# Kernel tuning notes

Measured on AMD Instinct MI355X. Metric: run time of the kernel, lower is better.

Reference implementation:

```python
import jax, jax.numpy as jnp
import numpy as np

N, E = 50000, 1600000
IN_F, OUT_F = 128, 128
T, B = 16, 8  # num_edge_types, num_bases
LN_EPS = 1e-5

def setup_inputs() -> dict:
    key = jax.random.key(0)
    ks = jax.random.split(key, 6)
    x = jax.random.normal(ks[0], (N, IN_F), dtype=jnp.float32)
    edge_index = jax.random.randint(ks[1], (2, E), 0, N, dtype=jnp.int64)
    edge_type = jax.random.randint(ks[2], (E,), 0, T, dtype=jnp.int64)
    edge_weight = jnp.ones((E,), dtype=jnp.float32)
    weight = jax.random.normal(ks[3], (B, IN_F, OUT_F), dtype=jnp.float32) * 0.05
    alpha = jax.random.normal(ks[4], (T, B), dtype=jnp.float32) * 0.05
    bias = jnp.zeros((OUT_F,), dtype=jnp.float32)
    w_self = jax.random.normal(ks[5], (IN_F, OUT_F), dtype=jnp.float32) * 0.05
    ln_gamma = jnp.ones((OUT_F,), dtype=jnp.float32)
    ln_beta = jnp.zeros((OUT_F,), dtype=jnp.float32)
    return {"x": x, "edge_index": edge_index, "edge_type": edge_type,
            "edge_weight": edge_weight, "weight": weight, "alpha": alpha,
            "bias": bias, "w_self": w_self, "ln_gamma": ln_gamma, "ln_beta": ln_beta}

def reference(x, edge_index, edge_type, edge_weight, weight, alpha, bias, w_self, ln_gamma, ln_beta):
    n = x.shape[0]
    row, col = edge_index[0], edge_index[1]
    # graph.row_norm(): normalize edge weights by destination-row weighted degree (full graph)
    deg = jax.ops.segment_sum(edge_weight, row, num_segments=n)
    norm_w = edge_weight / jnp.maximum(deg[row], 1e-12)
    # basis combination: W_t = sum_b alpha[t,b] * weight[b]
    W = jnp.einsum('tb,bio->tio', alpha, weight)            # [T, in, out]
    h_all = jnp.einsum('ni,tio->tno', x, W)                  # [T, N, out]
    # fused per-edge-type spmm: msg_e = norm_w_e * h_all[type_e, col_e], scatter-add to row_e
    msgs = h_all[edge_type, col] * norm_w[:, None]           # [E, out]
    h = jax.ops.segment_sum(msgs, row, num_segments=n)       # [N, out]
    # dropout is identity in eval mode; layer norm with affine params
    mu = jnp.mean(h, axis=-1, keepdims=True)
    var = jnp.mean((h - mu) ** 2, axis=-1, keepdims=True)
    h = (h - mu) * jax.lax.rsqrt(var + LN_EPS) * ln_gamma + ln_beta
    h = h + bias
    h = h + x @ w_self
    return h
```

## Files before the change

kernel.cpp:

```cpp
#include <hip/hip_runtime.h>

#define NT 16
#define NB 8
#define CAP 80
#define BUKCAP 8960
#define EPB 4096

typedef __attribute__((ext_vector_type(8))) short short8;
typedef __attribute__((ext_vector_type(4))) float f32x4;
typedef __attribute__((ext_vector_type(2))) float f32x2;

__device__ __forceinline__ unsigned short f2bf(float f) {
  unsigned int u = __float_as_uint(f);
  u += 0x7FFFu + ((u >> 16) & 1u);
  return (unsigned short)(u >> 16);
}
__device__ __forceinline__ unsigned int packbf2(float a, float b) {
  return (unsigned int)f2bf(a) | ((unsigned int)f2bf(b) << 16);
}

__device__ __forceinline__ f32x2 pk_mul(f32x2 a, f32x2 b) {
  f32x2 r;
  asm("v_pk_mul_f32 %0, %1, %2" : "=v"(r) : "v"(a), "v"(b));
  return r;
}
__device__ __forceinline__ void pk_fma_lo(f32x2& acc, f32x2 x, f32x2 c) {
  asm("v_pk_fma_f32 %0, %1, %2, %0 op_sel_hi:[1,0,1]" : "+v"(acc) : "v"(x), "v"(c));
}
__device__ __forceinline__ void pk_fma_hi(f32x2& acc, f32x2 x, f32x2 c) {
  asm("v_pk_fma_f32 %0, %1, %2, %0 op_sel:[0,1,0] op_sel_hi:[1,1,1]"
      : "+v"(acc) : "v"(x), "v"(c));
}

__device__ __forceinline__ void xprep_body(const float* __restrict__ x,
                                           unsigned short* __restrict__ xb, int i,
                                           int total8) {
  if (i < total8) {
    const float4* p = (const float4*)(x + (size_t)i * 8);
    float4 v0 = p[0], v1 = p[1];
    uint4 q = make_uint4(packbf2(v0.x, v0.y), packbf2(v0.z, v0.w),
                         packbf2(v1.x, v1.y), packbf2(v1.z, v1.w));
    *(uint4*)(xb + (size_t)i * 8) = q;
  }
}

__device__ __forceinline__ void wprep_body(const float* __restrict__ weight,
                                           const float* __restrict__ wself,
                                           unsigned short* __restrict__ WbB,
                                           unsigned short* __restrict__ wsB, int idx) {
  const int TOT = NB * 128 * 128;
  if (idx < TOT) {
    int b = idx >> 14, k = (idx >> 7) & 127, n = idx & 127;
    float s = weight[(size_t)(b * 128 + k) * 128 + n];
    int ct = n >> 4, n15 = n & 15, ks = k >> 5, lq = (k >> 3) & 3, j = k & 7;
    WbB[(size_t)((((b * 8 + ct) * 4 + ks) * 4 + lq) * 16 + n15) * 8 + j] = f2bf(s);
  } else if (idx < TOT + 128 * 128) {
    int i2 = idx - TOT;
    int k = i2 >> 7, n = i2 & 127;
    float s = wself[k * 128 + n];
    int ct = n >> 4, n15 = n & 15, ks = k >> 5, lq = (k >> 3) & 3, j = k & 7;
    wsB[((((ct * 4 + ks) * 4 + lq) * 16 + n15) * 8 + j)] = f2bf(s);
  }
}


__global__ __launch_bounds__(256) void k_part(
    const int* __restrict__ row, const int* __restrict__ col,
    const int* __restrict__ etype, const float* __restrict__ ew,
    int* __restrict__ gcount, int2* __restrict__ buk, const float* __restrict__ x,
    unsigned short* __restrict__ xb, const float* __restrict__ weight,
    const float* __restrict__ wself, unsigned short* __restrict__ WbB,
    unsigned short* __restrict__ wsB, int E, int N, int pb, int xbb) {
  int gb = blockIdx.x;
  if (gb < pb) {
    __shared__ int cnt[256];
    __shared__ int rbase[256];
    int base = gb * EPB;
    cnt[threadIdx.x] = 0;
    __syncthreads();
    int myb[16], myrank[16];
#pragma unroll
    for (int k = 0; k < 16; ++k) {
      int e = base + k * 256 + threadIdx.x;
      myb[k] = -1;
      myrank[k] = 0;
      if (e < E) {
        int r = row[e];
        int b = r >> 8;
        myb[k] = b | ((r & 255) << 8);
        myrank[k] = atomicAdd(&cnt[b], 1);
      }
    }
    __syncthreads();
    int c = cnt[threadIdx.x];
    rbase[threadIdx.x] = (c > 0) ? atomicAdd(&gcount[threadIdx.x], c) : 0;
    __syncthreads();
#pragma unroll
    for (int k = 0; k < 16; ++k) {
      if (myb[k] >= 0) {
        int e = base + k * 256 + threadIdx.x;
        int b = myb[k] & 255;
        int rl = (myb[k] >> 8) & 255;
        int pos = rbase[b] + myrank[k];
        if (pos < BUKCAP)
          buk[(size_t)b * BUKCAP + pos] =
              make_int2(col[e] | (etype[e] << 16) | (rl << 20), __float_as_int(ew[e]));
      }
    }
  } else if (gb < pb + xbb) {
    xprep_body(x, xb, (gb - pb) * 256 + threadIdx.x, N * 16);
  } else {
    wprep_body(weight, wself, WbB, wsB, (gb - pb - xbb) * 256 + threadIdx.x);
  }
}


__global__ __launch_bounds__(256) void k_bin(const int* __restrict__ gcount,
                                             const int2* __restrict__ buk,
                                             int* __restrict__ rcnt,
                                             int2* __restrict__ epk, int N) {
  __shared__ int cnt[256];
  int b = blockIdx.x;
  int n = gcount[b];
  if (n > BUKCAP) n = BUKCAP;
  cnt[threadIdx.x] = 0;
  __syncthreads();
  const int2* src = buk + (size_t)b * BUKCAP;
  for (int i = threadIdx.x; i < n; i += 256) {
    int2 rec = src[i];
    int lr = (rec.x >> 20) & 255;
    int pos = atomicAdd(&cnt[lr], 1);
    if (pos < CAP) {
      int grow = (b << 8) + lr;
      epk[(size_t)grow * CAP + pos] = make_int2(rec.x & 0xFFFFF, rec.y);
    }
  }
  __syncthreads();
  int grow = (b << 8) + threadIdx.x;
  if (grow < N) rcnt[grow] = min(cnt[threadIdx.x], CAP);
}


__global__ __launch_bounds__(256) void k_prep(
    const int* __restrict__ row, const int* __restrict__ col,
    const int* __restrict__ etype, const float* __restrict__ ew,
    int* __restrict__ rcnt, int2* __restrict__ epk, const float* __restrict__ x,
    unsigned short* __restrict__ xb, const float* __restrict__ weight,
    const float* __restrict__ wself, unsigned short* __restrict__ WbB,
    unsigned short* __restrict__ wsB, int E, int N, int eb, int xbb) {
  int gb = blockIdx.x;
  if (gb < eb) {
    int e0 = (gb * 256 + threadIdx.x) * 2;
    int e1 = e0 + 1;
    int r0 = -1, r1 = -1, pos0 = 0, pos1 = 0;
    if (e0 < E) { r0 = row[e0]; pos0 = atomicAdd(&rcnt[r0], 1); }
    if (e1 < E) { r1 = row[e1]; pos1 = atomicAdd(&rcnt[r1], 1); }
    if (r0 >= 0 && pos0 < CAP)
      epk[(size_t)r0 * CAP + pos0] = make_int2(col[e0] | (etype[e0] << 16),
                                               __float_as_int(ew[e0]));
    if (r1 >= 0 && pos1 < CAP)
      epk[(size_t)r1 * CAP + pos1] = make_int2(col[e1] | (etype[e1] << 16),
                                               __float_as_int(ew[e1]));
  } else if (gb < eb + xbb) {
    xprep_body(x, xb, (gb - eb) * 256 + threadIdx.x, N * 16);
  } else {
    wprep_body(weight, wself, WbB, wsB, (gb - eb - xbb) * 256 + threadIdx.x);
  }
}


__global__ void k_xprep(const float* __restrict__ x, unsigned short* __restrict__ xb,
                        int total8) {
  xprep_body(x, xb, blockIdx.x * 256 + threadIdx.x, total8);
}

__global__ void k_wprep(const float* __restrict__ weight, const float* __restrict__ wself,
                        unsigned short* __restrict__ WbB,
                        unsigned short* __restrict__ wselfB) {
  wprep_body(weight, wself, WbB, wselfB, blockIdx.x * 256 + threadIdx.x);
}

__global__ void k_count(const int* __restrict__ row, int* __restrict__ cnt, int E) {
  int e = blockIdx.x * blockDim.x + threadIdx.x;
  if (e < E) atomicAdd(&cnt[row[e]], 1);
}

__global__ __launch_bounds__(256) void k_scan_local(const int* __restrict__ cnt,
                                                    int* __restrict__ rstart,
                                                    int* __restrict__ bsum, int n) {
  __shared__ int ws[4];
  int tid = threadIdx.x;
  int i = blockIdx.x * 256 + tid;
  int lane = tid & 63, w = tid >> 6;
  int v = (i < n) ? cnt[i] : 0;
  int s = v;
#pragma unroll
  for (int d = 1; d < 64; d <<= 1) {
    int t = __shfl_up(s, d);
    if (lane >= d) s += t;
  }
  if (lane == 63) ws[w] = s;
  __syncthreads();
  int add = 0;
  for (int j = 0; j < w; ++j) add += ws[j];
  if (i < n) rstart[i] = s + add - v;
  if (tid == 255) bsum[blockIdx.x] = s + add;
}

__global__ __launch_bounds__(256) void k_scan_small(const int* __restrict__ bsum,
                                                    int* __restrict__ bsumx, int nb) {
  __shared__ int ws[4];
  int tid = threadIdx.x;
  int lane = tid & 63, w = tid >> 6;
  int v = (tid < nb) ? bsum[tid] : 0;
  int s = v;
#pragma unroll
  for (int d = 1; d < 64; d <<= 1) {
    int t = __shfl_up(s, d);
    if (lane >= d) s += t;
  }
  if (lane == 63) ws[w] = s;
  __syncthreads();
  int add = 0;
  for (int j = 0; j < w; ++j) add += ws[j];
  if (tid < nb) bsumx[tid] = s + add - v;
}

__global__ void k_scan_add(int* __restrict__ rstart, int* __restrict__ nxt,
                           const int* __restrict__ bsumx, int n) {
  int i = blockIdx.x * 256 + threadIdx.x;
  if (i < n) {
    int v = rstart[i] + bsumx[blockIdx.x];
    rstart[i] = v;
    nxt[i] = v;
  }
}

__global__ void k_scatter_csr(const int* __restrict__ row, const int* __restrict__ col,
                              const int* __restrict__ etype, const float* __restrict__ ew,
                              int* __restrict__ nxt, int2* __restrict__ epk, int E) {
  int e = blockIdx.x * blockDim.x + threadIdx.x;
  if (e < E) {
    int r = row[e];
    int pos = atomicAdd(&nxt[r], 1);
    epk[pos] = make_int2(col[e] | (etype[e] << 16), __float_as_int(ew[e]));
  }
}


__device__ __forceinline__ void edge_math(f32x2 xA, f32x2 xB, float wz,
                                          const float* alds, int t8, float& dsum,
                                          f32x2* acc0, f32x2* acc1) {
  dsum += wz;
  f32x4 aA = *(const f32x4*)(alds + t8);
  f32x4 aB = *(const f32x4*)(alds + t8 + 4);
  f32x2 wp = f32x2{wz, wz};
  f32x2 q01 = pk_mul(__builtin_shufflevector(aA, aA, 0, 1), wp);
  f32x2 q23 = pk_mul(__builtin_shufflevector(aA, aA, 2, 3), wp);
  f32x2 q45 = pk_mul(__builtin_shufflevector(aB, aB, 0, 1), wp);
  f32x2 q67 = pk_mul(__builtin_shufflevector(aB, aB, 2, 3), wp);
  pk_fma_lo(acc0[0], xA, q01); pk_fma_lo(acc1[0], xB, q01);
  pk_fma_hi(acc0[1], xA, q01); pk_fma_hi(acc1[1], xB, q01);
  pk_fma_lo(acc0[2], xA, q23); pk_fma_lo(acc1[2], xB, q23);
  pk_fma_hi(acc0[3], xA, q23); pk_fma_hi(acc1[3], xB, q23);
  pk_fma_lo(acc0[4], xA, q45); pk_fma_lo(acc1[4], xB, q45);
  pk_fma_hi(acc0[5], xA, q45); pk_fma_hi(acc1[5], xB, q45);
  pk_fma_lo(acc0[6], xA, q67); pk_fma_lo(acc1[6], xB, q67);
  pk_fma_hi(acc0[7], xA, q67); pk_fma_hi(acc1[7], xB, q67);
}

template <bool BF16X>
__device__ __forceinline__ void edge_tail(int2 p, float wz, const unsigned short* xb,
                                          const float* x, const float* alds, int fl,
                                          int N, float& dsum, f32x2* acc0, f32x2* acc1) {
  int c = p.x & 0xFFFF;
  c = (c < N) ? c : 0;
  int t8 = ((p.x >> 16) & 15) << 3;
  f32x2 xA, xB;
  if constexpr (BF16X) {
    uint2 u = *(const uint2*)(xb + ((size_t)c << 7) + fl * 4);
    xA = f32x2{__uint_as_float(u.x << 16), __uint_as_float(u.x & 0xFFFF0000u)};
    xB = f32x2{__uint_as_float(u.y << 16), __uint_as_float(u.y & 0xFFFF0000u)};
  } else {
    float4 v = *(const float4*)(x + ((size_t)c << 7) + fl * 4);
    xA = f32x2{v.x, v.y};
    xB = f32x2{v.z, v.w};
  }
  edge_math(xA, xB, wz, alds, t8, dsum, acc0, acc1);
}

template <bool BF16X>
__global__ __launch_bounds__(1024, 8) void k_main(
    const float* __restrict__ x, const unsigned short* __restrict__ xb,
    const int* __restrict__ rstart, const int* __restrict__ rcnt, int binned,
    const int2* __restrict__ epk, const float* __restrict__ alpha,
    const unsigned short* __restrict__ WbB, const unsigned short* __restrict__ wselfB,
    const float* __restrict__ gamma, const float* __restrict__ beta,
    const float* __restrict__ bias, float* __restrict__ out, int N) {
  __shared__ unsigned short g[NB * 2048];
  __shared__ float alds[NT * NB];
  __shared__ float2 stats[16][8];

  int tid = threadIdx.x;
  int lane = tid & 63;
  int wid = tid >> 6;
  int l15 = lane & 15, lq = lane >> 4;
  int fl = lane & 31;
  int half = lane >> 5;
  int rbase = blockIdx.x * 16;
  int r = rbase + wid;

  if (tid < NT * NB) alds[tid] = alpha[tid];
  __syncthreads();

  f32x2 acc0[NB], acc1[NB];
#pragma unroll
  for (int b = 0; b < NB; ++b) { acc0[b] = (f32x2)0.f; acc1[b] = (f32x2)0.f; }
  float dsum = 0.f;

  int sb = 0, d = 0;
  if (r < N) {
    d = rcnt[r];
    sb = binned ? r * CAP : rstart[r];
    if (binned && d > CAP) d = CAP;
  }

  const int2* ep = epk + sb + half;
  int e = 0;
  if (d >= 4) {
    int2 pa = ep[0], pb = ep[2];
    do {
      int2 pn0 = ep[4];
      int2 pn1 = ep[6];
      int ca = pa.x & 0xFFFF;
      int cb = pb.x & 0xFFFF;
      if constexpr (BF16X) {
        uint2 ua = *(const uint2*)(xb + ((size_t)ca << 7) + fl * 4);
        uint2 ub = *(const uint2*)(xb + ((size_t)cb << 7) + fl * 4);
        f32x2 aAx = f32x2{__uint_as_float(ua.x << 16), __uint_as_float(ua.x & 0xFFFF0000u)};
        f32x2 aBx = f32x2{__uint_as_float(ua.y << 16), __uint_as_float(ua.y & 0xFFFF0000u)};
        edge_math(aAx, aBx, __int_as_float(pa.y), alds, ((pa.x >> 16) & 15) << 3,
                  dsum, acc0, acc1);
        f32x2 bAx = f32x2{__uint_as_float(ub.x << 16), __uint_as_float(ub.x & 0xFFFF0000u)};
        f32x2 bBx = f32x2{__uint_as_float(ub.y << 16), __uint_as_float(ub.y & 0xFFFF0000u)};
        edge_math(bAx, bBx, __int_as_float(pb.y), alds, ((pb.x >> 16) & 15) << 3,
                  dsum, acc0, acc1);
      } else {
        float4 va = *(const float4*)(x + ((size_t)ca << 7) + fl * 4);
        float4 vb = *(const float4*)(x + ((size_t)cb << 7) + fl * 4);
        edge_math(f32x2{va.x, va.y}, f32x2{va.z, va.w}, __int_as_float(pa.y), alds,
                  ((pa.x >> 16) & 15) << 3, dsum, acc0, acc1);
        edge_math(f32x2{vb.x, vb.y}, f32x2{vb.z, vb.w}, __int_as_float(pb.y), alds,
                  ((pb.x >> 16) & 15) << 3, dsum, acc0, acc1);
      }
      pa = pn0;
      pb = pn1;
      ep += 4;
      e += 4;
    } while (e + 4 <= d);
  }
  for (; e + 2 <= d; e += 2, ep += 2) {
    int2 p = *ep;
    edge_tail<BF16X>(p, __int_as_float(p.y), xb, x, alds, fl, N, dsum, acc0, acc1);
  }
  if (e < d) {
    int2 p = *ep;
    float wz = half ? 0.f : __int_as_float(p.y);
    edge_tail<BF16X>(p, wz, xb, x, alds, fl, N, dsum, acc0, acc1);
  }

  dsum += __shfl_xor(dsum, 32);
#pragma unroll
  for (int b = 0; b < NB; ++b) {
    acc0[b].x += __shfl_xor(acc0[b].x, 32);
    acc0[b].y += __shfl_xor(acc0[b].y, 32);
    acc1[b].x += __shfl_xor(acc1[b].x, 32);
    acc1[b].y += __shfl_xor(acc1[b].y, 32);
  }
  float rdeg = 1.f / fmaxf(dsum, 1e-12f);
  int wofs = wid * 256 + ((fl * 8) ^ ((wid & 7) << 4));
  if (half == 0) {
#pragma unroll
    for (int b = 0; b < 4; ++b) {
      uint2 q = make_uint2(packbf2(acc0[b].x * rdeg, acc0[b].y * rdeg),
                           packbf2(acc1[b].x * rdeg, acc1[b].y * rdeg));
      *(uint2*)((char*)g + b * 4096 + wofs) = q;
    }
  } else {
#pragma unroll
    for (int i = 0; i < 4; ++i) {
      int b = 4 + i;
      uint2 q = make_uint2(packbf2(acc0[4 + i].x * rdeg, acc0[4 + i].y * rdeg),
                           packbf2(acc1[4 + i].x * rdeg, acc1[4 + i].y * rdeg));
      *(uint2*)((char*)g + b * 4096 + wofs) = q;
    }
  }
  __syncthreads();

  f32x4 accA = (f32x4)0.f, accS = (f32x4)0.f;
  if (wid < 8) {
    int ct = wid;
#pragma unroll
    for (int b = 0; b < NB; ++b) {
#pragma unroll
      for (int ks = 0; ks < 4; ++ks) {
        short8 av = *(const short8*)((const char*)g + b * 4096 + l15 * 256 +
                                     ((ks * 64 + lq * 16) ^ ((l15 & 7) << 4)));
        short8 bw = *(const short8*)(WbB +
            (size_t)(((b * 8 + ct) * 4 + ks) * 4 + lq) * 128 + l15 * 8);
        accA = __builtin_amdgcn_mfma_f32_16x16x32_bf16(av, bw, accA, 0, 0, 0);
      }
    }
    int rs_row = rbase + l15;
#pragma unroll
    for (int ks = 0; ks < 4; ++ks) {
      short8 av;
      if constexpr (BF16X) {
        if (rs_row < N)
          av = *(const short8*)(xb + ((size_t)rs_row << 7) + ks * 32 + lq * 8);
        else
          av = (short8)(short)0;
      } else {
        uint4 q = make_uint4(0u, 0u, 0u, 0u);
        if (rs_row < N) {
          const float* xp = x + ((size_t)rs_row << 7) + ks * 32 + lq * 8;
          float4 w0 = *(const float4*)xp;
          float4 w1 = *(const float4*)(xp + 4);
          q = make_uint4(packbf2(w0.x, w0.y), packbf2(w0.z, w0.w),
                         packbf2(w1.x, w1.y), packbf2(w1.z, w1.w));
        }
        av = *(short8*)&q;
      }
      short8 bw = *(const short8*)(wselfB + (size_t)((ct * 4 + ks) * 4 + lq) * 128 + l15 * 8);
      accS = __builtin_amdgcn_mfma_f32_16x16x32_bf16(av, bw, accS, 0, 0, 0);
    }
#pragma unroll
    for (int reg = 0; reg < 4; ++reg) {
      float v = accA[reg];
      float s1 = v, s2 = v * v;
#pragma unroll
      for (int m = 1; m < 16; m <<= 1) {
        s1 += __shfl_xor(s1, m);
        s2 += __shfl_xor(s2, m);
      }
      if (l15 == 0) stats[lq * 4 + reg][ct] = make_float2(s1, s2);
    }
  }
  __syncthreads();
  if (wid < 8) {
    int ct = wid;
    int c = ct * 16 + l15;
    float ga = gamma[c], be = beta[c], bi = bias[c];
#pragma unroll
    for (int reg = 0; reg < 4; ++reg) {
      int rowl = lq * 4 + reg;
      float S1 = 0.f, S2 = 0.f;
#pragma unroll
      for (int k2 = 0; k2 < 8; ++k2) {
        float2 p = stats[rowl][k2];
        S1 += p.x; S2 += p.y;
      }
      float mu = S1 * (1.f / 128.f);
      float var = S2 * (1.f / 128.f) - mu * mu;
      float rstd = rsqrtf(fmaxf(var, 0.f) + 1e-5f);
      int rg = rbase + rowl;
      if (rg < N)
        out[(size_t)rg * 128 + c] = (accA[reg] - mu) * rstd * ga + be + bi + accS[reg];
    }
  }
}

extern "C" void kernel_launch(void* const* d_in, const int* in_sizes, int n_in,
                              void* d_out, int out_size, void* d_ws, size_t ws_size,
                              hipStream_t stream) {
  const float* x = (const float*)d_in[0];
  const int* ei = (const int*)d_in[1];
  const int* etype = (const int*)d_in[2];
  const float* ew = (const float*)d_in[3];
  const float* weight = (const float*)d_in[4];
  const float* alpha = (const float*)d_in[5];
  const float* bias = (const float*)d_in[6];
  const float* wself = (const float*)d_in[7];
  const float* gamma = (const float*)d_in[8];
  const float* beta = (const float*)d_in[9];
  float* out = (float*)d_out;

  int N = in_sizes[0] / 128;
  int E = in_sizes[2];
  const int* row = ei;
  const int* col = ei + E;
  int NBUK = (N + 255) >> 8;

  auto au = [](size_t v) { return (v + 255) & ~(size_t)255; };
  size_t sz_xb = (size_t)N * 128 * 2;
  size_t sz_WbB = (size_t)NB * 128 * 128 * 2;
  size_t sz_wsB = (size_t)128 * 128 * 2;

  size_t t_gc = 0;
  size_t t_rcnt = au(1024);
  size_t t_epk = t_rcnt + au((size_t)N * 4);
  size_t t_buk = t_epk + au((size_t)N * CAP * 8 + 256);
  size_t t_xb = t_buk + au((size_t)NBUK * BUKCAP * 8);
  size_t t_WbB = t_xb + au(sz_xb);
  size_t t_wsB = t_WbB + au(sz_WbB);
  size_t need_2pass = t_wsB + au(sz_wsB);

  size_t b_rcnt = 0;
  size_t b_epk = au((size_t)N * 4);
  size_t b_xb = b_epk + au((size_t)N * CAP * 8 + 256);
  size_t b_WbB = b_xb + au(sz_xb);
  size_t b_wsB = b_WbB + au(sz_WbB);
  size_t need_binned = b_wsB + au(sz_wsB);

  size_t c_cnt = 0;
  size_t c_rstart = au((size_t)N * 4);
  size_t c_nxt = c_rstart + au((size_t)N * 4);
  size_t c_bsum = c_nxt + au((size_t)N * 4);
  size_t c_bsumx = c_bsum + 1024;
  size_t c_epk = c_bsumx + 1024;
  size_t c_xb = c_epk + au((size_t)E * 8 + 256);
  size_t c_WbB_x = c_xb + au(sz_xb);
  size_t need_csr_xb = c_WbB_x + au(sz_WbB) + au(sz_wsB);
  size_t c_WbB_nox = c_xb;

  char* ws = (char*)d_ws;
  int eb = (E + 255) / 256;
  int nb = (N + 255) / 256;
  int mb = (N + 15) / 16;
  int xbb = (N * 16 + 255) / 256;
  int wbb = (NB * 128 * 128 + 128 * 128 + 255) / 256;

  if (ws_size >= need_2pass && N <= 65536) {
    int* gcount = (int*)(ws + t_gc);
    int* rcnt = (int*)(ws + t_rcnt);
    int2* epk = (int2*)(ws + t_epk);
    int2* buk = (int2*)(ws + t_buk);
    unsigned short* xb = (unsigned short*)(ws + t_xb);
    unsigned short* WbB = (unsigned short*)(ws + t_WbB);
    unsigned short* wsB = (unsigned short*)(ws + t_wsB);
    hipMemsetAsync(gcount, 0, (size_t)NBUK * 4, stream);
    int pb = (E + EPB - 1) / EPB;
    k_part<<<pb + xbb + wbb, 256, 0, stream>>>(row, col, etype, ew, gcount, buk, x,
                                               xb, weight, wself, WbB, wsB, E, N, pb,
                                               xbb);
    k_bin<<<NBUK, 256, 0, stream>>>(gcount, buk, rcnt, epk, N);
    k_main<true><<<mb, 1024, 0, stream>>>(x, xb, rcnt, rcnt, 1, epk, alpha, WbB, wsB,
                                          gamma, beta, bias, out, N);
  } else if (ws_size >= need_binned) {
    int* rcnt = (int*)(ws + b_rcnt);
    int2* epk = (int2*)(ws + b_epk);
    unsigned short* xb = (unsigned short*)(ws + b_xb);
    unsigned short* WbB = (unsigned short*)(ws + b_WbB);
    unsigned short* wsB = (unsigned short*)(ws + b_wsB);
    hipMemsetAsync(rcnt, 0, (size_t)N * 4, stream);
    int eb2 = (E + 511) / 512;
    k_prep<<<eb2 + xbb + wbb, 256, 0, stream>>>(row, col, etype, ew, rcnt, epk, x, xb,
                                                weight, wself, WbB, wsB, E, N, eb2,
                                                xbb);
    k_main<true><<<mb, 1024, 0, stream>>>(x, xb, rcnt, rcnt, 1, epk, alpha, WbB, wsB,
                                          gamma, beta, bias, out, N);
  } else {
    bool have_xb = ws_size >= need_csr_xb;
    int* cnt = (int*)(ws + c_cnt);
    int* rstart = (int*)(ws + c_rstart);
    int* nxt = (int*)(ws + c_nxt);
    int* bsum = (int*)(ws + c_bsum);
    int* bsumx = (int*)(ws + c_bsumx);
    int2* epk = (int2*)(ws + c_epk);
    unsigned short* xb = (unsigned short*)(ws + c_xb);
    unsigned short* WbB = (unsigned short*)(ws + (have_xb ? c_WbB_x : c_WbB_nox));
    unsigned short* wsB = WbB + NB * 128 * 128;
    hipMemsetAsync(cnt, 0, (size_t)N * 4, stream);
    k_count<<<eb, 256, 0, stream>>>(row, cnt, E);
    k_scan_local<<<nb, 256, 0, stream>>>(cnt, rstart, bsum, N);
    k_scan_small<<<1, 256, 0, stream>>>(bsum, bsumx, nb);
    k_scan_add<<<nb, 256, 0, stream>>>(rstart, nxt, bsumx, N);
    k_scatter_csr<<<eb, 256, 0, stream>>>(row, col, etype, ew, nxt, epk, E);
    if (have_xb) k_xprep<<<xbb, 256, 0, stream>>>(x, xb, N * 16);
    k_wprep<<<wbb, 256, 0, stream>>>(weight, wself, WbB, wsB);
    if (have_xb)
      k_main<true><<<mb, 1024, 0, stream>>>(x, xb, rstart, cnt, 0, epk, alpha, WbB,
                                            wsB, gamma, beta, bias, out, N);
    else
      k_main<false><<<mb, 1024, 0, stream>>>(x, nullptr, rstart, cnt, 0, epk, alpha,
                                             WbB, wsB, gamma, beta, bias, out, N);
  }
}
```

Baseline: 221.5 us.

## Fuse bucket binning into main aggregation kernel via shared-memory bins

Removes the separate k_bin pass and its per-row epk/rcnt global arrays. Each block of the new k_mainf handles 16 rows of one 256-row bucket. It scans the whole bucket from the partition buffer, keeps only its 16 rows, and bins their edges into shared memory before doing aggregation, MFMA projection and layer norm. This saves a kernel launch and a global write/read round trip of the binned edges. In exchange, each bucket's records are re-read 16 times, once by each of its sub-blocks, and the blocks are mapped to buckets in a swizzled order.

After: 233.9 us. 1.06x slower.

```diff
diff --git a/kernel.cpp b/kernel.cpp
--- a/kernel.cpp
+++ b/kernel.cpp
@@ -115,29 +115,210 @@
 }
 
 
-__global__ __launch_bounds__(256) void k_bin(const int* __restrict__ gcount,
-                                             const int2* __restrict__ buk,
-                                             int* __restrict__ rcnt,
-                                             int2* __restrict__ epk, int N) {
-  __shared__ int cnt[256];
-  int b = blockIdx.x;
-  int n = gcount[b];
-  if (n > BUKCAP) n = BUKCAP;
-  cnt[threadIdx.x] = 0;
-  __syncthreads();
-  const int2* src = buk + (size_t)b * BUKCAP;
-  for (int i = threadIdx.x; i < n; i += 256) {
+__device__ __forceinline__ void edge_math(f32x2 xA, f32x2 xB, float wz,
+                                          const float* alds, int t8, float& dsum,
+                                          f32x2* acc0, f32x2* acc1) {
+  dsum += wz;
+  f32x4 aA = *(const f32x4*)(alds + t8);
+  f32x4 aB = *(const f32x4*)(alds + t8 + 4);
+  f32x2 wp = f32x2{wz, wz};
+  f32x2 q01 = pk_mul(__builtin_shufflevector(aA, aA, 0, 1), wp);
+  f32x2 q23 = pk_mul(__builtin_shufflevector(aA, aA, 2, 3), wp);
+  f32x2 q45 = pk_mul(__builtin_shufflevector(aB, aB, 0, 1), wp);
+  f32x2 q67 = pk_mul(__builtin_shufflevector(aB, aB, 2, 3), wp);
+  pk_fma_lo(acc0[0], xA, q01); pk_fma_lo(acc1[0], xB, q01);
+  pk_fma_hi(acc0[1], xA, q01); pk_fma_hi(acc1[1], xB, q01);
+  pk_fma_lo(acc0[2], xA, q23); pk_fma_lo(acc1[2], xB, q23);
+  pk_fma_hi(acc0[3], xA, q23); pk_fma_hi(acc1[3], xB, q23);
+  pk_fma_lo(acc0[4], xA, q45); pk_fma_lo(acc1[4], xB, q45);
+  pk_fma_hi(acc0[5], xA, q45); pk_fma_hi(acc1[5], xB, q45);
+  pk_fma_lo(acc0[6], xA, q67); pk_fma_lo(acc1[6], xB, q67);
+  pk_fma_hi(acc0[7], xA, q67); pk_fma_hi(acc1[7], xB, q67);
+}
+
+
+__global__ __launch_bounds__(1024, 8) void k_mainf(
+    const float* __restrict__ x, const unsigned short* __restrict__ xb,
+    const int* __restrict__ gcount, const int2* __restrict__ buk,
+    const float* __restrict__ alpha, const unsigned short* __restrict__ WbB,
+    const unsigned short* __restrict__ wselfB, const float* __restrict__ gamma,
+    const float* __restrict__ beta, const float* __restrict__ bias,
+    float* __restrict__ out, int N, int NBUK) {
+  __shared__ unsigned short g[NB * 2048];
+  __shared__ float alds[NT * NB];
+  __shared__ float2 stats[16][8];
+  __shared__ int2 bins[16][CAP + 8];
+  __shared__ int bcnt[16];
+
+  int p = blockIdx.x;
+  int bucket = (p & 7) + 8 * (p >> 7);
+  int sub = (p >> 3) & 15;
+  if (bucket >= NBUK) return;
+  int rbase = bucket * 256 + sub * 16;
+
+  int tid = threadIdx.x;
+  int lane = tid & 63;
+  int wid = tid >> 6;
+  int l15 = lane & 15, lq = lane >> 4;
+  int fl = lane & 31;
+  int half = lane >> 5;
+  int r = rbase + wid;
+
+  if (tid < NT * NB) alds[tid] = alpha[tid];
+  if (tid < 16) bcnt[tid] = 0;
+  __syncthreads();
+
+  int n = min(gcount[bucket], BUKCAP);
+  const int2* src = buk + (size_t)bucket * BUKCAP;
+  for (int i = tid; i < n; i += 1024) {
     int2 rec = src[i];
     int lr = (rec.x >> 20) & 255;
-    int pos = atomicAdd(&cnt[lr], 1);
-    if (pos < CAP) {
-      int grow = (b << 8) + lr;
-      epk[(size_t)grow * CAP + pos] = make_int2(rec.x & 0xFFFFF, rec.y);
-    }
-  }
-  __syncthreads();
-  int grow = (b << 8) + threadIdx.x;
-  if (grow < N) rcnt[grow] = min(cnt[threadIdx.x], CAP);
+    if ((lr >> 4) == sub) {
+      int r16 = lr & 15;
+      int pos = atomicAdd(&bcnt[r16], 1);
+      if (pos < CAP) bins[r16][pos] = make_int2(rec.x & 0xFFFFF, rec.y);
+    }
+  }
+  __syncthreads();
+
+  f32x2 acc0[NB], acc1[NB];
+#pragma unroll
+  for (int b = 0; b < NB; ++b) { acc0[b] = (f32x2)0.f; acc1[b] = (f32x2)0.f; }
+  float dsum = 0.f;
+
+  int d = min(bcnt[wid], CAP);
+  const int2* ep = &bins[wid][half];
+  int e = 0;
+  if (d >= 4) {
+    int2 pa = ep[0], pb = ep[2];
+    do {
+      int2 pn0 = ep[4];
+      int2 pn1 = ep[6];
+      int ca = pa.x & 0xFFFF;
+      int cb = pb.x & 0xFFFF;
+      uint2 ua = *(const uint2*)(xb + ((size_t)ca << 7) + fl * 4);
+      uint2 ub = *(const uint2*)(xb + ((size_t)cb << 7) + fl * 4);
+      f32x2 aAx = f32x2{__uint_as_float(ua.x << 16), __uint_as_float(ua.x & 0xFFFF0000u)};
+      f32x2 aBx = f32x2{__uint_as_float(ua.y << 16), __uint_as_float(ua.y & 0xFFFF0000u)};
+      edge_math(aAx, aBx, __int_as_float(pa.y), alds, ((pa.x >> 16) & 15) << 3,
+                dsum, acc0, acc1);
+      f32x2 bAx = f32x2{__uint_as_float(ub.x << 16), __uint_as_float(ub.x & 0xFFFF0000u)};
+      f32x2 bBx = f32x2{__uint_as_float(ub.y << 16), __uint_as_float(ub.y & 0xFFFF0000u)};
+      edge_math(bAx, bBx, __int_as_float(pb.y), alds, ((pb.x >> 16) & 15) << 3,
+                dsum, acc0, acc1);
+      pa = pn0;
+      pb = pn1;
+      ep += 4;
+      e += 4;
+    } while (e + 4 <= d);
+  }
+  for (; e + 2 <= d; e += 2, ep += 2) {
+    int2 p2 = *ep;
+    int c = p2.x & 0xFFFF;
+    uint2 u = *(const uint2*)(xb + ((size_t)c << 7) + fl * 4);
+    f32x2 xA = f32x2{__uint_as_float(u.x << 16), __uint_as_float(u.x & 0xFFFF0000u)};
+    f32x2 xB = f32x2{__uint_as_float(u.y << 16), __uint_as_float(u.y & 0xFFFF0000u)};
+    edge_math(xA, xB, __int_as_float(p2.y), alds, ((p2.x >> 16) & 15) << 3, dsum,
+              acc0, acc1);
+  }
+  if (e < d) {
+    int2 p2 = *ep;
+    float wz = half ? 0.f : __int_as_float(p2.y);
+    int c = p2.x & 0xFFFF;
+    c = (c < N) ? c : 0;
+    uint2 u = *(const uint2*)(xb + ((size_t)c << 7) + fl * 4);
+    f32x2 xA = f32x2{__uint_as_float(u.x << 16), __uint_as_float(u.x & 0xFFFF0000u)};
+    f32x2 xB = f32x2{__uint_as_float(u.y << 16), __uint_as_float(u.y & 0xFFFF0000u)};
+    edge_math(xA, xB, wz, alds, ((p2.x >> 16) & 15) << 3, dsum, acc0, acc1);
+  }
+
+  dsum += __shfl_xor(dsum, 32);
+#pragma unroll
+  for (int b = 0; b < NB; ++b) {
+    acc0[b].x += __shfl_xor(acc0[b].x, 32);
+    acc0[b].y += __shfl_xor(acc0[b].y, 32);
+    acc1[b].x += __shfl_xor(acc1[b].x, 32);
+    acc1[b].y += __shfl_xor(acc1[b].y, 32);
+  }
+  float rdeg = 1.f / fmaxf(dsum, 1e-12f);
+  int wofs = wid * 256 + ((fl * 8) ^ ((wid & 7) << 4));
+  if (half == 0) {
+#pragma unroll
+    for (int b = 0; b < 4; ++b) {
+      uint2 q = make_uint2(packbf2(acc0[b].x * rdeg, acc0[b].y * rdeg),
+                           packbf2(acc1[b].x * rdeg, acc1[b].y * rdeg));
+      *(uint2*)((char*)g + b * 4096 + wofs) = q;
+    }
+  } else {
+#pragma unroll
+    for (int i = 0; i < 4; ++i) {
+      int b = 4 + i;
+      uint2 q = make_uint2(packbf2(acc0[4 + i].x * rdeg, acc0[4 + i].y * rdeg),
+                           packbf2(acc1[4 + i].x * rdeg, acc1[4 + i].y * rdeg));
+      *(uint2*)((char*)g + b * 4096 + wofs) = q;
+    }
+  }
+  __syncthreads();
+
+  f32x4 accA = (f32x4)0.f, accS = (f32x4)0.f;
+  if (wid < 8) {
+    int ct = wid;
+#pragma unroll
+    for (int b = 0; b < NB; ++b) {
+#pragma unroll
+      for (int ks = 0; ks < 4; ++ks) {
+        short8 av = *(const short8*)((const char*)g + b * 4096 + l15 * 256 +
+                                     ((ks * 64 + lq * 16) ^ ((l15 & 7) << 4)));
+        short8 bw = *(const short8*)(WbB +
+            (size_t)(((b * 8 + ct) * 4 + ks) * 4 + lq) * 128 + l15 * 8);
+        accA = __builtin_amdgcn_mfma_f32_16x16x32_bf16(av, bw, accA, 0, 0, 0);
+      }
+    }
+    int rs_row = rbase + l15;
+#pragma unroll
+    for (int ks = 0; ks < 4; ++ks) {
+      short8 av;
+      if (rs_row < N)
+        av = *(const short8*)(xb + ((size_t)rs_row << 7) + ks * 32 + lq * 8);
+      else
+        av = (short8)(short)0;
+      short8 bw = *(const short8*)(wselfB + (size_t)((ct * 4 + ks) * 4 + lq) * 128 + l15 * 8);
+      accS = __builtin_amdgcn_mfma_f32_16x16x32_bf16(av, bw, accS, 0, 0, 0);
+    }
+#pragma unroll
+    for (int reg = 0; reg < 4; ++reg) {
+      float v = accA[reg];
+      float s1 = v, s2 = v * v;
+#pragma unroll
+      for (int m = 1; m < 16; m <<= 1) {
+        s1 += __shfl_xor(s1, m);
+        s2 += __shfl_xor(s2, m);
+      }
+      if (l15 == 0) stats[lq * 4 + reg][ct] = make_float2(s1, s2);
+    }
+  }
+  __syncthreads();
+  if (wid < 8) {
+    int ct = wid;
+    int c = ct * 16 + l15;
+    float ga = gamma[c], be = beta[c], bi = bias[c];
+#pragma unroll
+    for (int reg = 0; reg < 4; ++reg) {
+      int rowl = lq * 4 + reg;
+      float S1 = 0.f, S2 = 0.f;
+#pragma unroll
+      for (int k2 = 0; k2 < 8; ++k2) {
+        float2 pp = stats[rowl][k2];
+        S1 += pp.x; S2 += pp.y;
+      }
+      float mu = S1 * (1.f / 128.f);
+      float var = S2 * (1.f / 128.f) - mu * mu;
+      float rstd = rsqrtf(fmaxf(var, 0.f) + 1e-5f);
+      int rg = rbase + rowl;
+      if (rg < N)
+        out[(size_t)rg * 128 + c] = (accA[reg] - mu) * rstd * ga + be + bi + accS[reg];
+    }
+  }
 }
 
 
@@ -247,27 +428,6 @@
   }
 }
 
-
-__device__ __forceinline__ void edge_math(f32x2 xA, f32x2 xB, float wz,
-                                          const float* alds, int t8, float& dsum,
-                                          f32x2* acc0, f32x2* acc1) {
-  dsum += wz;
-  f32x4 aA = *(const f32x4*)(alds + t8);
-  f32x4 aB = *(const f32x4*)(alds + t8 + 4);
-  f32x2 wp = f32x2{wz, wz};
-  f32x2 q01 = pk_mul(__builtin_shufflevector(aA, aA, 0, 1), wp);
-  f32x2 q23 = pk_mul(__builtin_shufflevector(aA, aA, 2, 3), wp);
-  f32x2 q45 = pk_mul(__builtin_shufflevector(aB, aB, 0, 1), wp);
-  f32x2 q67 = pk_mul(__builtin_shufflevector(aB, aB, 2, 3), wp);
-  pk_fma_lo(acc0[0], xA, q01); pk_fma_lo(acc1[0], xB, q01);
-  pk_fma_hi(acc0[1], xA, q01); pk_fma_hi(acc1[1], xB, q01);
-  pk_fma_lo(acc0[2], xA, q23); pk_fma_lo(acc1[2], xB, q23);
-  pk_fma_hi(acc0[3], xA, q23); pk_fma_hi(acc1[3], xB, q23);
-  pk_fma_lo(acc0[4], xA, q45); pk_fma_lo(acc1[4], xB, q45);
-  pk_fma_hi(acc0[5], xA, q45); pk_fma_hi(acc1[5], xB, q45);
-  pk_fma_lo(acc0[6], xA, q67); pk_fma_lo(acc1[6], xB, q67);
-  pk_fma_hi(acc0[7], xA, q67); pk_fma_hi(acc1[7], xB, q67);
-}
 
 template <bool BF16X>
 __device__ __forceinline__ void edge_tail(int2 p, float wz, const unsigned short* xb,
@@ -496,14 +656,12 @@
   size_t sz_WbB = (size_t)NB * 128 * 128 * 2;
   size_t sz_wsB = (size_t)128 * 128 * 2;
 
-  size_t t_gc = 0;
-  size_t t_rcnt = au(1024);
-  size_t t_epk = t_rcnt + au((size_t)N * 4);
-  size_t t_buk = t_epk + au((size_t)N * CAP * 8 + 256);
-  size_t t_xb = t_buk + au((size_t)NBUK * BUKCAP * 8);
-  size_t t_WbB = t_xb + au(sz_xb);
-  size_t t_wsB = t_WbB + au(sz_WbB);
-  size_t need_2pass = t_wsB + au(sz_wsB);
+  size_t f_gc = 0;
+  size_t f_buk = au((size_t)NBUK * 4);
+  size_t f_xb = f_buk + au((size_t)NBUK * BUKCAP * 8);
+  size_t f_WbB = f_xb + au(sz_xb);
+  size_t f_wsB = f_WbB + au(sz_WbB);
+  size_t need_fused = f_wsB + au(sz_wsB);
 
   size_t b_rcnt = 0;
   size_t b_epk = au((size_t)N * 4);
@@ -530,23 +688,21 @@
   int xbb = (N * 16 + 255) / 256;
   int wbb = (NB * 128 * 128 + 128 * 128 + 255) / 256;
 
-  if (ws_size >= need_2pass && N <= 65536) {
-    int* gcount = (int*)(ws + t_gc);
-    int* rcnt = (int*)(ws + t_rcnt);
-    int2* epk = (int2*)(ws + t_epk);
-    int2* buk = (int2*)(ws + t_buk);
-    unsigned short* xb = (unsigned short*)(ws + t_xb);
-    unsigned short* WbB = (unsigned short*)(ws + t_WbB);
-    unsigned short* wsB = (unsigned short*)(ws + t_wsB);
+  if (ws_size >= need_fused && N <= 65536) {
+    int* gcount = (int*)(ws + f_gc);
+    int2* buk = (int2*)(ws + f_buk);
+    unsigned short* xb = (unsigned short*)(ws + f_xb);
+    unsigned short* WbB = (unsigned short*)(ws + f_WbB);
+    unsigned short* wsB = (unsigned short*)(ws + f_wsB);
     hipMemsetAsync(gcount, 0, (size_t)NBUK * 4, stream);
     int pb = (E + EPB - 1) / EPB;
     k_part<<<pb + xbb + wbb, 256, 0, stream>>>(row, col, etype, ew, gcount, buk, x,
                                                xb, weight, wself, WbB, wsB, E, N, pb,
                                                xbb);
-    k_bin<<<NBUK, 256, 0, stream>>>(gcount, buk, rcnt, epk, N);
-    k_main<true><<<mb, 1024, 0, stream>>>(x, xb, rcnt, rcnt, 1, epk, alpha, WbB, wsB,
-                                          gamma, beta, bias, out, N);
-  } else if (ws_size >= need_binned) {
+    int gx = 128 * ((NBUK + 7) / 8);
+    k_mainf<<<gx, 1024, 0, stream>>>(x, xb, gcount, buk, alpha, WbB, wsB, gamma,
+                                     beta, bias, out, N, NBUK);
+  } else if (ws_size >= need_binned && N <= 65536) {
     int* rcnt = (int*)(ws + b_rcnt);
     int2* epk = (int2*)(ws + b_epk);
     unsigned short* xb = (unsigned short*)(ws + b_xb);
```
